# Performance work log

Hardware: AMD Instinct MI355X
Metric: run time of the kernel (lower is better)

The kernel has to match this reference:

```python
import jax, jax.numpy as jnp
import numpy as np

N_HEADS = 16
LN_EPS = 1e-5

def layer_norm(x, w):
    # matches torch LayerNorm in fp32, weight-only (no bias)
    x = x.astype(jnp.float32)
    mu = jnp.mean(x, axis=-1, keepdims=True)
    var = jnp.mean((x - mu) ** 2, axis=-1, keepdims=True)
    return (x - mu) / jnp.sqrt(var + LN_EPS) * w

def rotate_half(t):
    t1, t2 = jnp.split(t, 2, axis=-1)
    return jnp.concatenate((-t2, t1), axis=-1)

def setup_inputs() -> dict:
    key = jax.random.key(0)
    ks = jax.random.split(key, 16)
    B, S, D, C = 2, 2048, 1024, 1024
    H = N_HEADS
    hd = D // H
    # rotary tables: emb = cat(freqs, freqs), freqs = t * inv_freq
    inv_freq = 1.0 / (10000.0 ** (np.arange(0, hd, 2, dtype=np.float32) / hd))
    t = np.arange(S, dtype=np.float32)
    freqs = np.outer(t, inv_freq)                       # [S, hd/2]
    emb = np.concatenate([freqs, freqs], axis=-1)       # [S, hd]
    s = 0.02
    return {
        "x": jax.random.normal(ks[0], (B, S, D), jnp.float32),
        "rotary_cos": jnp.asarray(np.cos(emb)),
        "rotary_sin": jnp.asarray(np.sin(emb)),
        "c": jax.random.normal(ks[1], (B, C), jnp.float32),
        "norm1_w": jnp.ones((D,), jnp.float32),
        "qkv_w": jax.random.normal(ks[2], (3 * D, D), jnp.float32) * s,
        "out_w": jax.random.normal(ks[3], (D, D), jnp.float32) * s,
        "norm2_w": jnp.ones((D,), jnp.float32),
        "fc1_w": jax.random.normal(ks[4], (4 * D, D), jnp.float32) * s,
        "fc1_b": jnp.zeros((4 * D,), jnp.float32),
        "fc2_w": jax.random.normal(ks[5], (D, 4 * D), jnp.float32) * s,
        "fc2_b": jnp.zeros((D,), jnp.float32),
        # NOTE: module zero-inits adaLN; random here for a non-degenerate baseline
        "ada_w": jax.random.normal(ks[6], (6 * D, C), jnp.float32) * s,
        "ada_b": jnp.zeros((6 * D,), jnp.float32),
    }

def reference(x, rotary_cos, rotary_sin, c, norm1_w, qkv_w, out_w, norm2_w,
              fc1_w, fc1_b, fc2_w, fc2_b, ada_w, ada_b):
    B, S, D = x.shape
    H = N_HEADS
    hd = D // H
    # AdaLN conditioning -> six [B,1,D] modulation tensors
    mods = (c @ ada_w.T + ada_b)[:, None, :]                       # [B,1,6D]
    shift_msa, scale_msa, gate_msa, shift_mlp, scale_mlp, gate_mlp = jnp.split(mods, 6, axis=2)
    x_skip = x
    # LN + modulate + QKV
    h = layer_norm(x, norm1_w) * (1.0 + scale_msa) + shift_msa     # [B,S,D]
    qkv = (h @ qkv_w.T).reshape(B, S, 3, H, hd)
    # rotary applied to packed qkv (q, k, and v) as in the torchscript fallback
    cos = rotary_cos[None, :, None, None, :]                       # [1,S,1,1,hd]
    sin = rotary_sin[None, :, None, None, :]
    qkv = qkv * cos + rotate_half(qkv) * sin
    q, k, v = qkv[:, :, 0], qkv[:, :, 1], qkv[:, :, 2]             # [B,S,H,hd]
    scale = hd ** -0.5
    scores = jnp.einsum('bqhd,bkhd->bhqk', q, k) * scale           # [B,H,S,S]
    attn = jax.nn.softmax(scores, axis=-1)
    o = jnp.einsum('bhqk,bkhd->bqhd', attn, v).reshape(B, S, D)
    # gated residual (dropout=0 / eval)
    x = gate_msa * (o @ out_w.T) + x_skip
    # second LN + modulate + MLP (exact gelu, matching F.gelu default)
    h2 = layer_norm(x, norm2_w) * (1.0 + scale_mlp) + shift_mlp
    mlp = jax.nn.gelu(h2 @ fc1_w.T + fc1_b, approximate=False) @ fc2_w.T + fc2_b
    return gate_mlp * mlp + x
```

## Files before the change

kernel.cpp:

```cpp
#include <hip/hip_runtime.h>
#include <hip/hip_bf16.h>


typedef unsigned short u16;
typedef unsigned int   u32;
typedef __bf16 bf16x8 __attribute__((ext_vector_type(8)));
typedef float  f32x4  __attribute__((ext_vector_type(4)));

#define MFMA_BF16(a, b, c) __builtin_amdgcn_mfma_f32_16x16x32_bf16((a), (b), (c), 0, 0, 0)

__device__ __forceinline__ float b2f(u16 u) {
    union { u32 i; float f; } v; v.i = ((u32)u) << 16; return v.f;
}
__device__ __forceinline__ u16 f2b(float f) {
    union { u32 i; float f; } v; v.f = f;
    u32 i = v.i;
    return (u16)((i + 0x7FFFu + ((i >> 16) & 1u)) >> 16);
}
__device__ __forceinline__ u32 pk2(float a, float b) {
#if __has_builtin(__builtin_amdgcn_cvt_pk_bf16_f32)
    typedef __bf16 bf16x2_t __attribute__((ext_vector_type(2)));
    union { bf16x2_t v; u32 u; } cv;
    cv.v = __builtin_amdgcn_cvt_pk_bf16_f32(a, b);
    return cv.u;
#else
    return (u32)f2b(a) | ((u32)f2b(b) << 16);
#endif
}
__device__ __forceinline__ float finz(float v) {
    return __builtin_isfinite(v) ? v : 0.0f;
}
__device__ __forceinline__ void dma16(const void* g, void* l) {
    __builtin_amdgcn_global_load_lds(
        (const __attribute__((address_space(1))) unsigned int*)(uintptr_t)g,
        (__attribute__((address_space(3))) unsigned int*)(uintptr_t)l,
        16, 0, 0);
}

__global__ __launch_bounds__(256) void convert_kernel(
    const float* __restrict__ in, u16* __restrict__ out, int n8, int kshift)
{
    int i = blockIdx.x * 256 + threadIdx.x;
    if (i >= n8) return;
    size_t o = (size_t)i * 8;
    int bk   = (int)(o >> (kshift + 7));
    int rem  = (int)(o & (((size_t)128 << kshift) - 1));
    int kg   = rem >> 10;
    int nloc = (rem >> 3) & 127;
    const float* src = in + (((size_t)bk * 128 + nloc) << kshift) + kg * 8;
    float4 a = *(const float4*)src;
    float4 b = *(const float4*)(src + 4);
    union { u16 s[8]; float4 v; } wp;
    wp.s[0] = f2b(a.x); wp.s[1] = f2b(a.y); wp.s[2] = f2b(a.z); wp.s[3] = f2b(a.w);
    wp.s[4] = f2b(b.x); wp.s[5] = f2b(b.y); wp.s[6] = f2b(b.z); wp.s[7] = f2b(b.w);
    *(float4*)(out + o) = wp.v;
}

__global__ __launch_bounds__(64) void mods_kernel(
    const float* __restrict__ c, const float* __restrict__ ada_w,
    const float* __restrict__ ada_b, float* __restrict__ mods)
{
    const int n = blockIdx.x;
    const int lane = threadIdx.x;
    const float* wr = ada_w + (size_t)n * 1024;
    float a0 = 0.f, a1 = 0.f;
    for (int k = lane; k < 1024; k += 64) {
        float w = wr[k];
        a0 += w * c[k];
        a1 += w * c[1024 + k];
    }
    for (int o = 32; o > 0; o >>= 1) {
        a0 += __shfl_down(a0, o, 64);
        a1 += __shfl_down(a1, o, 64);
    }
    if (lane == 0) {
        float bb = ada_b[n];
        mods[n]        = a0 + bb;
        mods[6144 + n] = a1 + bb;
    }
}

__global__ __launch_bounds__(256) void ln_mod_kernel(
    const u16* __restrict__ xbf, const float* __restrict__ xf,
    const float* __restrict__ w, const float* __restrict__ mods,
    int scale_off, int shift_off, u16* __restrict__ out)
{
    const int row = blockIdx.x;
    const int b   = row >> 11;
    const int tid = threadIdx.x;
    const size_t base = (size_t)row * 1024 + tid * 4;
    float v[4];
    if (xf) {
        float4 t = *(const float4*)(xf + base);
        v[0] = t.x; v[1] = t.y; v[2] = t.z; v[3] = t.w;
    } else {
        uint2 p = *(const uint2*)(xbf + base);
        union { u32 i; float f; } a, bb, cc, d;
        a.i  = p.x << 16;          v[0] = a.f;
        bb.i = p.x & 0xFFFF0000u;  v[1] = bb.f;
        cc.i = p.y << 16;          v[2] = cc.f;
        d.i  = p.y & 0xFFFF0000u;  v[3] = d.f;
    }
    float s  = v[0] + v[1] + v[2] + v[3];
    float sq = v[0]*v[0] + v[1]*v[1] + v[2]*v[2] + v[3]*v[3];
    __shared__ float rs[256], rq[256];
    rs[tid] = s; rq[tid] = sq;
    __syncthreads();
    for (int o = 128; o > 0; o >>= 1) {
        if (tid < o) { rs[tid] += rs[tid + o]; rq[tid] += rq[tid + o]; }
        __syncthreads();
    }
    const float mean = rs[0] * (1.0f / 1024.0f);
    const float var  = rq[0] * (1.0f / 1024.0f) - mean * mean;
    const float inv  = rsqrtf(fmaxf(var, 0.f) + 1e-5f);
    union { u16 s4[4]; uint2 u2; } pk;
    for (int i = 0; i < 4; ++i) {
        int cidx = tid * 4 + i;
        float y = (v[i] - mean) * inv * w[cidx];
        y = y * (1.0f + mods[b * 6144 + scale_off + cidx]) + mods[b * 6144 + shift_off + cidx];
        pk.s4[i] = f2b(y);
    }
    size_t o = ((size_t)(row >> 7)) * 131072 + ((tid * 4) >> 3) * 1024
             + (row & 127) * 8 + ((tid * 4) & 7);
    *(uint2*)(out + o) = pk.u2;
}

template<int MODE>
__global__ __launch_bounds__(256) void gemm128(
    const u16* __restrict__ A, const u16* __restrict__ W,
    int M, int N, int K,
    const float* __restrict__ mods, const float* __restrict__ bias,
    const float* __restrict__ resid_f, const u16* __restrict__ resid_bf,
    float* __restrict__ out_f, u16* __restrict__ out_bf,
    u16* __restrict__ aux1, u16* __restrict__ aux2,
    const float* __restrict__ rcos, const float* __restrict__ rsin)
{
    __shared__ u16 As[3][4096];
    __shared__ u16 Bs[3][4096];
    const int tid  = threadIdx.x;
    const int wave = tid >> 6, lane = tid & 63;
    const int quad = lane >> 4, l15 = lane & 15;
    const int wi = wave >> 1, wj = wave & 1;
    const int m0 = blockIdx.y * 128, n0 = blockIdx.x * 128;

    f32x4 acc[4][4] = {};

    const u16* Asrc = A + (size_t)m0 * K + wave * 1024 + lane * 8;
    const u16* Bsrc = W + (size_t)n0 * K + wave * 1024 + lane * 8;
    const int wo = wave * 1024;

    auto stage = [&](int tt, int buf) {
        const u16* a = Asrc + (size_t)tt * 4096;
        const u16* b = Bsrc + (size_t)tt * 4096;
        dma16(a,       &As[buf][wo]);
        dma16(a + 512, &As[buf][wo + 512]);
        dma16(b,       &Bs[buf][wo]);
        dma16(b + 512, &Bs[buf][wo + 512]);
    };

    const int nt = K >> 5;
    stage(0, 0);
    stage(1, 1);

    int cur = 0;
    for (int t = 0; t < nt; ++t) {
        if (t + 1 < nt) {
            __asm volatile("s_waitcnt vmcnt(4)" ::: "memory");
        } else {
            __asm volatile("s_waitcnt vmcnt(0)" ::: "memory");
        }
        __builtin_amdgcn_s_barrier();
        if (t + 2 < nt) {
            int nb = cur + 2; if (nb >= 3) nb -= 3;
            stage(t + 2, nb);
        }
        bf16x8 af[4], bw[4];
        #pragma unroll
        for (int f = 0; f < 4; ++f) {
            af[f] = *(const bf16x8*)(&As[cur][quad * 1024 + (wi * 64 + f * 16 + l15) * 8]);
            bw[f] = *(const bf16x8*)(&Bs[cur][quad * 1024 + (wj * 64 + f * 16 + l15) * 8]);
        }
        #pragma unroll
        for (int fi = 0; fi < 4; ++fi)
            #pragma unroll
            for (int fj = 0; fj < 4; ++fj)
                acc[fi][fj] = MFMA_BF16(af[fi], bw[fj], acc[fi][fj]);
        cur = (cur + 1 == 3) ? 0 : cur + 1;
    }

    if (MODE == 4) {
        const int colbase = n0 + wj * 64;
        const int wcol = colbase >> 10;
        const int hh   = (colbase & 1023) >> 6;
        #pragma unroll
        for (int fi = 0; fi < 4; ++fi) {
            const int rbase = m0 + wi * 64 + fi * 16 + quad * 4;
            #pragma unroll
            for (int reg = 0; reg < 4; ++reg) {
                const int r = rbase + reg;
                const int b = r >> 11, s = r & 2047;
                const int bh = b * 16 + hh;
                #pragma unroll
                for (int fj = 0; fj < 2; ++fj) {
                    const int d2 = fj * 16 + l15;
                    float va = acc[fi][fj][reg];
                    float vb = acc[fi][fj + 2][reg];
                    float ca = rcos[s * 64 + d2];
                    float sa = rsin[s * 64 + d2];
                    float ra = va * ca - vb * sa;
                    float rb = vb * ca + va * sa;
                    if (wcol == 0) {
                        ra *= 0.125f; rb *= 0.125f;
                        u16* dst = aux1 + ((size_t)bh * 2048 + s) * 64;
                        dst[d2]      = f2b(ra);
                        dst[d2 + 32] = f2b(rb);
                    } else if (wcol == 1) {
                        size_t base = (size_t)bh * 131072 + (s >> 6) * 4096
                                    + (s & 63) * 8 + (d2 & 7);
                        aux2[base + (d2 >> 3) * 512]        = f2b(ra);
                        aux2[base + ((d2 >> 3) + 4) * 512]  = f2b(rb);
                    } else {
                        size_t base = (size_t)bh * 131072 + (s >> 6) * 4096
                                    + ((s & 63) >> 3) * 512 + (s & 7);
                        out_bf[base + d2 * 8]        = f2b(ra);
                        out_bf[base + (d2 + 32) * 8] = f2b(rb);
                    }
                }
            }
        }
        return;
    }

    #pragma unroll
    for (int fi = 0; fi < 4; ++fi) {
        #pragma unroll
        for (int fj = 0; fj < 4; ++fj) {
            const int cidx  = n0 + wj * 64 + fj * 16 + l15;
            const int rbase = m0 + wi * 64 + fi * 16 + quad * 4;
            #pragma unroll
            for (int reg = 0; reg < 4; ++reg) {
                const int r = rbase + reg;
                float v = acc[fi][fj][reg];
                if (MODE == 1) {
                    float u = v + bias[cidx];
                    float g = 0.5f * u * (1.0f + erff(u * 0.70710678118654752f));
                    size_t o = ((size_t)(r >> 7)) * 524288 + (cidx >> 3) * 1024
                             + (r & 127) * 8 + (cidx & 7);
                    out_bf[o] = f2b(g);
                } else if (MODE == 2) {
                    int bb = r >> 11;
                    float gate = mods[bb * 6144 + 2048 + cidx];
                    out_bf[(size_t)r * N + cidx] = f2b(gate * v + resid_f[(size_t)r * N + cidx]);
                } else if (MODE == 3) {
                    int bb = r >> 11;
                    float u = v + bias[cidx];
                    float gate = mods[bb * 6144 + 5120 + cidx];
                    out_f[(size_t)r * N + cidx] =
                        finz(gate * u + b2f(resid_bf[(size_t)r * N + cidx]));
                }
            }
        }
    }
}

__global__ __launch_bounds__(256) void attn_kernel(
    const u16* __restrict__ Q, const u16* __restrict__ Kb,
    const u16* __restrict__ Vb, u16* __restrict__ O)
{
    __shared__ u16 Ks[4096];
    __shared__ u16 Vs[4096];
    __shared__ u16 Ps[4][16 * 72];
    const int tid  = threadIdx.x;
    const int wave = tid >> 6, lane = tid & 63;
    const int quad = lane >> 4, l15 = lane & 15;
    const int bh = blockIdx.x & 31, qt = blockIdx.x >> 5;

    const u16* Qh = Q  + ((size_t)bh * 2048 + qt * 64) * 64;
    const u16* Kh = Kb + (size_t)bh * 131072;
    const u16* Vh = Vb + (size_t)bh * 131072;

    bf16x8 aq[2];
    #pragma unroll
    for (int kh = 0; kh < 2; ++kh)
        aq[kh] = *(const bf16x8*)(Qh + (size_t)(wave * 16 + l15) * 64 + kh * 32 + quad * 8);

    f32x4 acc_o[4] = {};
    float lsum[4] = {0.f, 0.f, 0.f, 0.f};

    for (int kb = 0; kb < 32; ++kb) {
        __syncthreads();
        const u16* kc = Kh + kb * 4096;
        const u16* vc = Vh + kb * 4096;
        dma16(kc + (2 * wave) * 512 + lane * 8,     &Ks[(2 * wave) * 512]);
        dma16(kc + (2 * wave + 1) * 512 + lane * 8, &Ks[(2 * wave + 1) * 512]);
        dma16(vc + (2 * wave) * 512 + lane * 8,     &Vs[(2 * wave) * 512]);
        dma16(vc + (2 * wave + 1) * 512 + lane * 8, &Vs[(2 * wave + 1) * 512]);
        __syncthreads();

        f32x4 sc[4] = {};
        #pragma unroll
        for (int kt = 0; kt < 4; ++kt)
            #pragma unroll
            for (int kh = 0; kh < 2; ++kh) {
                bf16x8 bk = *(const bf16x8*)(&Ks[(quad + kh * 4) * 512 + (kt * 16 + l15) * 8]);
                sc[kt] = MFMA_BF16(aq[kh], bk, sc[kt]);
            }

        #pragma unroll
        for (int kt = 0; kt < 4; ++kt)
            #pragma unroll
            for (int reg = 0; reg < 4; ++reg)
                sc[kt][reg] = __expf(fminf(sc[kt][reg], 50.f));
        #pragma unroll
        for (int reg = 0; reg < 4; ++reg)
            lsum[reg] += (sc[0][reg] + sc[1][reg]) + (sc[2][reg] + sc[3][reg]);

        #pragma unroll
        for (int kt = 0; kt < 4; kt += 2)
            #pragma unroll
            for (int reg = 0; reg < 4; ++reg) {
                u32 p = pk2(sc[kt][reg], sc[kt + 1][reg]);
                Ps[wave][(quad * 4 + reg) * 72 + kt * 16 + l15]       = (u16)p;
                Ps[wave][(quad * 4 + reg) * 72 + (kt + 1) * 16 + l15] = (u16)(p >> 16);
            }
        __asm volatile("s_waitcnt lgkmcnt(0)" ::: "memory");

        bf16x8 ap0 = *(const bf16x8*)(&Ps[wave][l15 * 72 + quad * 8]);
        bf16x8 ap1 = *(const bf16x8*)(&Ps[wave][l15 * 72 + 32 + quad * 8]);
        #pragma unroll
        for (int dt = 0; dt < 4; ++dt) {
            bf16x8 bv0 = *(const bf16x8*)(&Vs[quad * 512 + (dt * 16 + l15) * 8]);
            bf16x8 bv1 = *(const bf16x8*)(&Vs[(quad + 4) * 512 + (dt * 16 + l15) * 8]);
            acc_o[dt] = MFMA_BF16(ap0, bv0, acc_o[dt]);
            acc_o[dt] = MFMA_BF16(ap1, bv1, acc_o[dt]);
        }
    }

    float linv[4];
    #pragma unroll
    for (int reg = 0; reg < 4; ++reg) {
        float l = lsum[reg];
        l += __shfl_xor(l, 1, 64);
        l += __shfl_xor(l, 2, 64);
        l += __shfl_xor(l, 4, 64);
        l += __shfl_xor(l, 8, 64);
        linv[reg] = 1.0f / l;
    }

    const int b = bh >> 4, hh = bh & 15;
    #pragma unroll
    for (int dt = 0; dt < 4; ++dt)
        #pragma unroll
        for (int reg = 0; reg < 4; ++reg) {
            int q = qt * 64 + wave * 16 + quad * 4 + reg;
            int r = b * 2048 + q;
            int col = hh * 64 + dt * 16 + l15;
            float v = acc_o[dt][reg] * linv[reg];
            O[((size_t)(r >> 7)) * 131072 + (col >> 3) * 1024
              + (r & 127) * 8 + (col & 7)] = f2b(v);
        }
}

extern "C" void kernel_launch(void* const* d_in, const int* in_sizes, int n_in,
                              void* d_out, int out_size, void* d_ws, size_t ws_size,
                              hipStream_t stream)
{
    const float* x     = (const float*)d_in[0];
    const float* rcos  = (const float*)d_in[1];
    const float* rsin  = (const float*)d_in[2];
    const float* c     = (const float*)d_in[3];
    const float* n1w   = (const float*)d_in[4];
    const float* qkvw  = (const float*)d_in[5];
    const float* outw  = (const float*)d_in[6];
    const float* n2w   = (const float*)d_in[7];
    const float* fc1w  = (const float*)d_in[8];
    const float* fc1b  = (const float*)d_in[9];
    const float* fc2w  = (const float*)d_in[10];
    const float* fc2b  = (const float*)d_in[11];
    const float* adaw  = (const float*)d_in[12];
    const float* adab  = (const float*)d_in[13];
    float* out = (float*)d_out;

    char* ws = (char*)d_ws;
    const size_t MB8 = (size_t)8 * 1024 * 1024;
    float* mods  = (float*)ws;
    u16*   W     = (u16*)(ws + 49152);
    char*  S1    = ws + 49152 + MB8;
    char*  S2    = S1 + MB8;

    u16* h    = (u16*)d_out;
    u16* qs   = (u16*)S1;
    u16* ks   = (u16*)S2;
    u16* vT   = (u16*)(S2 + MB8);
    u16* ob   = (u16*)d_out;
    u16* x2   = (u16*)S1;
    u16* h2   = (u16*)d_out;
    u16* mid  = (u16*)S2;

    mods_kernel<<<6144, 64, 0, stream>>>(c, adaw, adab, mods);
    ln_mod_kernel<<<4096, 256, 0, stream>>>(nullptr, x, n1w, mods, 1024, 0, h);
    convert_kernel<<<1536, 256, 0, stream>>>(qkvw, W, 393216, 10);
    gemm128<4><<<dim3(24, 32), 256, 0, stream>>>(h, W, 4096, 3072, 1024,
        nullptr, nullptr, nullptr, nullptr, nullptr, vT, qs, ks, rcos, rsin);
    attn_kernel<<<1024, 256, 0, stream>>>(qs, ks, vT, ob);
    convert_kernel<<<512, 256, 0, stream>>>(outw, W, 131072, 10);
    gemm128<2><<<dim3(8, 32), 256, 0, stream>>>(ob, W, 4096, 1024, 1024,
        mods, nullptr, x, nullptr, nullptr, x2, nullptr, nullptr, nullptr, nullptr);
    ln_mod_kernel<<<4096, 256, 0, stream>>>(x2, nullptr, n2w, mods, 4096, 3072, h2);
    convert_kernel<<<2048, 256, 0, stream>>>(fc1w, W, 524288, 10);
    gemm128<1><<<dim3(32, 32), 256, 0, stream>>>(h2, W, 4096, 4096, 1024,
        nullptr, fc1b, nullptr, nullptr, nullptr, mid, nullptr, nullptr, nullptr, nullptr);
    convert_kernel<<<2048, 256, 0, stream>>>(fc2w, W, 524288, 12);
    gemm128<3><<<dim3(8, 32), 256, 0, stream>>>(mid, W, 4096, 1024, 4096,
        mods, fc2b, nullptr, x2, out, nullptr, nullptr, nullptr, nullptr, nullptr);
}
```

Baseline: 421.8 us.

## Double-buffer K/V tiles in attention kernel with async prefetch

The attention kernel now keeps two shared-memory buffers for K and V and prefetches the next key block with DMA while computing on the current one. Explicit vmcnt waits and raw barriers replace the two __syncthreads per iteration, and s_setprio is raised around the MFMA sections. The goal is to hide global-memory load latency behind the QK and PV matrix math. In exchange, shared-memory use per block doubles for K/V, which can lower occupancy, and correctness now relies on the vmcnt(4) count matching the number of outstanding DMA loads.

New measurement: 446.9 us. 1.06x slower.

```diff
diff --git a/kernel.cpp b/kernel.cpp
--- a/kernel.cpp
+++ b/kernel.cpp
@@ -267,8 +267,8 @@
     const u16* __restrict__ Q, const u16* __restrict__ Kb,
     const u16* __restrict__ Vb, u16* __restrict__ O)
 {
-    __shared__ u16 Ks[4096];
-    __shared__ u16 Vs[4096];
+    __shared__ u16 Ks[2][4096];
+    __shared__ u16 Vs[2][4096];
     __shared__ u16 Ps[4][16 * 72];
     const int tid  = threadIdx.x;
     const int wave = tid >> 6, lane = tid & 63;
@@ -279,6 +279,15 @@
     const u16* Kh = Kb + (size_t)bh * 131072;
     const u16* Vh = Vb + (size_t)bh * 131072;
 
+    auto stageKV = [&](int kb, int buf) {
+        const u16* kc = Kh + kb * 4096;
+        const u16* vc = Vh + kb * 4096;
+        dma16(kc + (2 * wave) * 512 + lane * 8,     &Ks[buf][(2 * wave) * 512]);
+        dma16(kc + (2 * wave + 1) * 512 + lane * 8, &Ks[buf][(2 * wave + 1) * 512]);
+        dma16(vc + (2 * wave) * 512 + lane * 8,     &Vs[buf][(2 * wave) * 512]);
+        dma16(vc + (2 * wave + 1) * 512 + lane * 8, &Vs[buf][(2 * wave + 1) * 512]);
+    };
+
     bf16x8 aq[2];
     #pragma unroll
     for (int kh = 0; kh < 2; ++kh)
@@ -287,24 +296,28 @@
     f32x4 acc_o[4] = {};
     float lsum[4] = {0.f, 0.f, 0.f, 0.f};
 
+    stageKV(0, 0);
+
     for (int kb = 0; kb < 32; ++kb) {
-        __syncthreads();
-        const u16* kc = Kh + kb * 4096;
-        const u16* vc = Vh + kb * 4096;
-        dma16(kc + (2 * wave) * 512 + lane * 8,     &Ks[(2 * wave) * 512]);
-        dma16(kc + (2 * wave + 1) * 512 + lane * 8, &Ks[(2 * wave + 1) * 512]);
-        dma16(vc + (2 * wave) * 512 + lane * 8,     &Vs[(2 * wave) * 512]);
-        dma16(vc + (2 * wave + 1) * 512 + lane * 8, &Vs[(2 * wave + 1) * 512]);
-        __syncthreads();
+        const int cur = kb & 1;
+        if (kb + 1 < 32) {
+            stageKV(kb + 1, cur ^ 1);
+            __asm volatile("s_waitcnt vmcnt(4)" ::: "memory");
+        } else {
+            __asm volatile("s_waitcnt vmcnt(0)" ::: "memory");
+        }
+        __builtin_amdgcn_s_barrier();
 
         f32x4 sc[4] = {};
+        __builtin_amdgcn_s_setprio(1);
         #pragma unroll
         for (int kt = 0; kt < 4; ++kt)
             #pragma unroll
             for (int kh = 0; kh < 2; ++kh) {
-                bf16x8 bk = *(const bf16x8*)(&Ks[(quad + kh * 4) * 512 + (kt * 16 + l15) * 8]);
+                bf16x8 bk = *(const bf16x8*)(&Ks[cur][(quad + kh * 4) * 512 + (kt * 16 + l15) * 8]);
                 sc[kt] = MFMA_BF16(aq[kh], bk, sc[kt]);
             }
+        __builtin_amdgcn_s_setprio(0);
 
         #pragma unroll
         for (int kt = 0; kt < 4; ++kt)
@@ -327,13 +340,18 @@
 
         bf16x8 ap0 = *(const bf16x8*)(&Ps[wave][l15 * 72 + quad * 8]);
         bf16x8 ap1 = *(const bf16x8*)(&Ps[wave][l15 * 72 + 32 + quad * 8]);
+        __builtin_amdgcn_s_setprio(1);
         #pragma unroll
         for (int dt = 0; dt < 4; ++dt) {
-            bf16x8 bv0 = *(const bf16x8*)(&Vs[quad * 512 + (dt * 16 + l15) * 8]);
-            bf16x8 bv1 = *(const bf16x8*)(&Vs[(quad + 4) * 512 + (dt * 16 + l15) * 8]);
+            bf16x8 bv0 = *(const bf16x8*)(&Vs[cur][quad * 512 + (dt * 16 + l15) * 8]);
+            bf16x8 bv1 = *(const bf16x8*)(&Vs[cur][(quad + 4) * 512 + (dt * 16 + l15) * 8]);
             acc_o[dt] = MFMA_BF16(ap0, bv0, acc_o[dt]);
             acc_o[dt] = MFMA_BF16(ap1, bv1, acc_o[dt]);
         }
+        __builtin_amdgcn_s_setprio(0);
+
+        __asm volatile("s_waitcnt lgkmcnt(0)" ::: "memory");
+        __builtin_amdgcn_s_barrier();
     }
 
     float linv[4];
```
